# Performance work log

Hardware: AMD Instinct MI355X
Metric: run time of the kernel (lower is better)

The kernel has to match this reference:

```python
import jax, jax.numpy as jnp
import numpy as np

N_SIDE = 14          # ViT-S/16 on 224x224 -> 14x14 patches
D_BACKBONE = 384
D_MODEL = 512
B_CLIPS = 32
T_FRAMES = 64
BT = B_CLIPS * T_FRAMES
LN_EPS = 1e-5


def setup_inputs() -> dict:
    key = jax.random.key(0)
    k0, k1, k2, k3, k4 = jax.random.split(key, 5)
    patch_tokens = jax.random.normal(k0, (BT, N_SIDE * N_SIDE, D_BACKBONE), dtype=jnp.float32)
    raw = jax.random.uniform(k1, (BT, 4), dtype=jnp.float32)
    # make well-formed boxes: x1<=x2, y1<=y2 (module clamps anyway)
    xy1 = jnp.minimum(raw[:, :2], raw[:, 2:])
    xy2 = jnp.maximum(raw[:, :2], raw[:, 2:])
    bboxes = jnp.concatenate([xy1, xy2], axis=1)
    obj_visible = jax.random.bernoulli(k2, 0.9, (BT,)).astype(jnp.float32)
    W = jax.random.normal(k3, (D_BACKBONE, D_MODEL), dtype=jnp.float32) * 0.02
    b = jnp.zeros((D_MODEL,), dtype=jnp.float32)
    gamma = jnp.ones((D_MODEL,), dtype=jnp.float32)
    beta = jnp.zeros((D_MODEL,), dtype=jnp.float32)
    mask_token = jax.random.normal(k4, (1, D_MODEL), dtype=jnp.float32) * 0.02
    return {"patch_tokens": patch_tokens, "bboxes": bboxes, "obj_visible": obj_visible,
            "B": B_CLIPS, "T": T_FRAMES, "W": W, "b": b, "gamma": gamma, "beta": beta,
            "mask_token": mask_token}


def _roi_mean_pool(patch_tokens, bboxes):
    bt, N, D = patch_tokens.shape
    n = N_SIDE
    grid = patch_tokens.reshape(bt, n, n, D)
    # exact replica of torch index math (clamp -> trunc/ceil -> clamp -> max)
    x1 = jnp.clip(bboxes[:, 0] * n, 0, n - 1).astype(jnp.int32)
    y1 = jnp.clip(bboxes[:, 1] * n, 0, n - 1).astype(jnp.int32)
    x2 = jnp.clip(jnp.ceil(jnp.clip(bboxes[:, 2] * n, 0, n)), 1, n).astype(jnp.int32)
    y2 = jnp.clip(jnp.ceil(jnp.clip(bboxes[:, 3] * n, 0, n)), 1, n).astype(jnp.int32)
    x2 = jnp.maximum(x2, x1 + 1)
    y2 = jnp.maximum(y2, y1 + 1)
    idx = jnp.arange(n)
    my = (idx[None, :] >= y1[:, None]) & (idx[None, :] < y2[:, None])  # [BT, n]
    mx = (idx[None, :] >= x1[:, None]) & (idx[None, :] < x2[:, None])  # [BT, n]
    mask = (my[:, :, None] & mx[:, None, :]).astype(grid.dtype)        # [BT, n, n]
    count = ((y2 - y1) * (x2 - x1)).astype(grid.dtype)                 # >= 1 always
    pooled = jnp.einsum('bhw,bhwd->bd', mask, grid) / count[:, None]
    return pooled


def reference(patch_tokens, bboxes, obj_visible, B, T, W, b, gamma, beta, mask_token):
    pooled = _roi_mean_pool(patch_tokens, bboxes)          # [BT, D_backbone]
    out = pooled @ W + b                                   # [BT, d_model]
    mu = jnp.mean(out, axis=-1, keepdims=True)
    var = jnp.mean(jnp.square(out - mu), axis=-1, keepdims=True)
    out = (out - mu) * jax.lax.rsqrt(var + LN_EPS) * gamma + beta
    vis = obj_visible[:, None]
    out = vis * out + (1.0 - vis) * mask_token             # learnable mask token blend
    return out.reshape(B, T, -1)
```

## Files before the change

### kernel.cpp

```cpp
#include <hip/hip_runtime.h>
#include <hip/hip_bf16.h>

#define N_SIDE 14
#define N_PATCH (N_SIDE * N_SIDE)
#define D_BB 384
#define DQ_BB (D_BB / 4)
#define D_MODEL 512
#define CQ (D_MODEL / 4)
#define BT_TOTAL 2048
#define LN_EPS 1e-5f
#define PGROUPS 8

#define GROWS 8
#define GKP 8
#define GKCHUNK (D_BB / GKP)

__device__ __forceinline__ void fma4(float4& a, float s, const float4& wv) {
    a.x = fmaf(s, wv.x, a.x);
    a.y = fmaf(s, wv.y, a.y);
    a.z = fmaf(s, wv.z, a.z);
    a.w = fmaf(s, wv.w, a.w);
}

__device__ __forceinline__ void add4(float4& a, const float4& b) {
    a.x += b.x; a.y += b.y; a.z += b.z; a.w += b.w;
}

__device__ __forceinline__ void box_params(const float* __restrict__ bboxes, int bt,
                                           int& x1, int& y1, int& wd, int& total) {
    const float bx1 = bboxes[bt * 4 + 0];
    const float by1 = bboxes[bt * 4 + 1];
    const float bx2 = bboxes[bt * 4 + 2];
    const float by2 = bboxes[bt * 4 + 3];
    x1 = (int)fminf(fmaxf(bx1 * (float)N_SIDE, 0.f), (float)(N_SIDE - 1));
    y1 = (int)fminf(fmaxf(by1 * (float)N_SIDE, 0.f), (float)(N_SIDE - 1));
    int x2 = (int)fminf(fmaxf(ceilf(fminf(fmaxf(bx2 * (float)N_SIDE, 0.f), (float)N_SIDE)), 1.f), (float)N_SIDE);
    int y2 = (int)fminf(fmaxf(ceilf(fminf(fmaxf(by2 * (float)N_SIDE, 0.f), (float)N_SIDE)), 1.f), (float)N_SIDE);
    x2 = max(x2, x1 + 1);
    y2 = max(y2, y1 + 1);
    wd = x2 - x1;
    total = wd * (y2 - y1);
}

__global__ __launch_bounds__(768) void pool_kernel(
    const float* __restrict__ patch,
    const float* __restrict__ bboxes,
    float* __restrict__ pooled)
{
    const int bt = blockIdx.x;
    const int t  = threadIdx.x;
    const int qd = t % DQ_BB;
    const int g  = t / DQ_BB;

    int x1, y1, wd, total;
    box_params(bboxes, bt, x1, y1, wd, total);
    const float inv_count = 1.f / (float)total;
    const float inv_wd = 1.f / (float)wd;
    const int cell0 = y1 * N_SIDE + x1;

    const float4* __restrict__ base = (const float4*)patch + (size_t)bt * N_PATCH * DQ_BB + qd;

    auto cell_off = [&](int c) -> size_t {
        const int y = (int)(((float)c + 0.5f) * inv_wd);
        const int x = c - y * wd;
        return (size_t)(cell0 + y * N_SIDE + x) * DQ_BB;
    };

    float4 acc = make_float4(0.f, 0.f, 0.f, 0.f);
    int c = g;
    for (; c + 3 * PGROUPS < total; c += 4 * PGROUPS) {
        const float4 v0 = base[cell_off(c)];
        const float4 v1 = base[cell_off(c + PGROUPS)];
        const float4 v2 = base[cell_off(c + 2 * PGROUPS)];
        const float4 v3 = base[cell_off(c + 3 * PGROUPS)];
        acc.x += (v0.x + v1.x) + (v2.x + v3.x);
        acc.y += (v0.y + v1.y) + (v2.y + v3.y);
        acc.z += (v0.z + v1.z) + (v2.z + v3.z);
        acc.w += (v0.w + v1.w) + (v2.w + v3.w);
    }
    for (; c < total; c += PGROUPS) {
        const float4 v = base[cell_off(c)];
        acc.x += v.x; acc.y += v.y; acc.z += v.z; acc.w += v.w;
    }

    __shared__ float4 part[PGROUPS][DQ_BB];
    part[g][qd] = acc;
    __syncthreads();

    if (t < DQ_BB) {
        float4 s = part[0][t];
#pragma unroll
        for (int p = 1; p < PGROUPS; ++p) add4(s, part[p][t]);
        s.x *= inv_count; s.y *= inv_count; s.z *= inv_count; s.w *= inv_count;
        ((float4*)pooled)[(size_t)bt * DQ_BB + t] = s;
    }
}

__global__ __launch_bounds__(1024) void gemm_ln_kernel(
    const float* __restrict__ pooled,
    const float* __restrict__ W,
    const float* __restrict__ bias,
    const float* __restrict__ gamma,
    const float* __restrict__ beta,
    const float* __restrict__ mask_tok,
    const float* __restrict__ vis,
    float* __restrict__ out)
{
    const int tid = threadIdx.x;
    const int lq  = tid & 63;
    const int w   = tid >> 6;
    const int h   = w & 1;
    const int p   = w >> 1;
    const int r0  = blockIdx.x * GROWS;

    __shared__ float4 red4[4][GROWS][CQ];
    __shared__ float  lnred[2][GROWS][2];

    const int hq = h * 64 + lq;
    const int dbase = __builtin_amdgcn_readfirstlane(p * GKCHUNK);

    const float4* Wq = (const float4*)W;
    const float*  A  = pooled + (size_t)r0 * D_BB;

    float4 acc[GROWS];
#pragma unroll
    for (int r = 0; r < GROWS; ++r) acc[r] = make_float4(0.f, 0.f, 0.f, 0.f);

#pragma unroll 2
    for (int i = 0; i < GKCHUNK / 4; ++i) {
        const int d = dbase + i * 4;
        const float4 w0 = Wq[(size_t)(d + 0) * CQ + hq];
        const float4 w1 = Wq[(size_t)(d + 1) * CQ + hq];
        const float4 w2 = Wq[(size_t)(d + 2) * CQ + hq];
        const float4 w3 = Wq[(size_t)(d + 3) * CQ + hq];
#pragma unroll
        for (int r = 0; r < GROWS; ++r) {
            const float* Ar = A + r * D_BB + d;
            const float a0 = Ar[0];
            const float a1 = Ar[1];
            const float a2 = Ar[2];
            const float a3 = Ar[3];
            fma4(acc[r], a0, w0);
            fma4(acc[r], a1, w1);
            fma4(acc[r], a2, w2);
            fma4(acc[r], a3, w3);
        }
    }

    if (p >= 4) {
#pragma unroll
        for (int r = 0; r < GROWS; ++r) red4[p - 4][r][hq] = acc[r];
    }
    __syncthreads();
    if (p < 4) {
#pragma unroll
        for (int r = 0; r < GROWS; ++r) add4(acc[r], red4[p][r][hq]);
    }
    __syncthreads();
    if (p == 2 || p == 3) {
#pragma unroll
        for (int r = 0; r < GROWS; ++r) red4[p - 2][r][hq] = acc[r];
    }
    __syncthreads();
    if (p < 2) {
#pragma unroll
        for (int r = 0; r < GROWS; ++r) add4(acc[r], red4[p][r][hq]);
    }
    __syncthreads();
    if (p == 1) {
#pragma unroll
        for (int r = 0; r < GROWS; ++r) red4[0][r][hq] = acc[r];
    }
    __syncthreads();

    if (p == 0) {
        const float4 bj = ((const float4*)bias)[hq];
#pragma unroll
        for (int r = 0; r < GROWS; ++r) {
            add4(acc[r], red4[0][r][hq]);
            add4(acc[r], bj);
            float s  = acc[r].x + acc[r].y + acc[r].z + acc[r].w;
            float s2 = acc[r].x * acc[r].x + acc[r].y * acc[r].y +
                       acc[r].z * acc[r].z + acc[r].w * acc[r].w;
#pragma unroll
            for (int off = 32; off >= 1; off >>= 1) {
                s  += __shfl_xor(s,  off);
                s2 += __shfl_xor(s2, off);
            }
            if (lq == 0) { lnred[h][r][0] = s; lnred[h][r][1] = s2; }
        }
    }
    __syncthreads();

    if (p == 0) {
        const float4 g4 = ((const float4*)gamma)[hq];
        const float4 b4 = ((const float4*)beta)[hq];
        const float4 m4 = ((const float4*)mask_tok)[hq];
#pragma unroll
        for (int r = 0; r < GROWS; ++r) {
            const float s    = lnred[0][r][0] + lnred[1][r][0];
            const float s2   = lnred[0][r][1] + lnred[1][r][1];
            const float mean = s * (1.f / (float)D_MODEL);
            const float var  = s2 * (1.f / (float)D_MODEL) - mean * mean;
            const float rstd = rsqrtf(var + LN_EPS);
            const float v    = vis[r0 + r];
            const float iv   = 1.f - v;
            float4 o;
            o.x = v * ((acc[r].x - mean) * rstd * g4.x + b4.x) + iv * m4.x;
            o.y = v * ((acc[r].y - mean) * rstd * g4.y + b4.y) + iv * m4.y;
            o.z = v * ((acc[r].z - mean) * rstd * g4.z + b4.z) + iv * m4.z;
            o.w = v * ((acc[r].w - mean) * rstd * g4.w + b4.w) + iv * m4.w;
            ((float4*)out)[(size_t)(r0 + r) * CQ + hq] = o;
        }
    }
}

extern "C" void kernel_launch(void* const* d_in, const int* in_sizes, int n_in,
                              void* d_out, int out_size, void* d_ws, size_t ws_size,
                              hipStream_t stream) {
    const float* patch  = (const float*)d_in[0];
    const float* bboxes = (const float*)d_in[1];
    const float* vis    = (const float*)d_in[2];
    const float* W      = (const float*)d_in[5];
    const float* bias   = (const float*)d_in[6];
    const float* gamma  = (const float*)d_in[7];
    const float* beta   = (const float*)d_in[8];
    const float* mtok   = (const float*)d_in[9];

    float* pooled = (float*)d_ws;
    float* out    = (float*)d_out;

    pool_kernel<<<BT_TOTAL, 768, 0, stream>>>(patch, bboxes, pooled);
    gemm_ln_kernel<<<BT_TOTAL / GROWS, 1024, 0, stream>>>(
        pooled, W, bias, gamma, beta, mtok, vis, out);
}
```

Measured before the change: 36.46 us.

## Replace FP32 GEMM+LN with bf16 MFMA kernel using prepacked weights

Swaps the scalar FP32 FMA projection for a bf16 MFMA 16x16x32 kernel. The pool kernel now writes pooled features as bf16, and its first 64 blocks also convert and pack W into MFMA B-fragment layout, which adds work to those blocks. The LayerNorm reduction now uses a per-wave shuffle plus a small cross-wave shared-memory step instead of the multi-stage shared-memory split-K reduction. This cuts GEMM compute and the pooled and W traffic, at the cost of bf16 rounding on the inputs and a less coalesced scalar output store.

```diff
diff --git a/kernel.cpp b/kernel.cpp
--- a/kernel.cpp
+++ b/kernel.cpp
@@ -6,20 +6,18 @@
 #define D_BB 384
 #define DQ_BB (D_BB / 4)
 #define D_MODEL 512
-#define CQ (D_MODEL / 4)
 #define BT_TOTAL 2048
 #define LN_EPS 1e-5f
 #define PGROUPS 8
-
-#define GROWS 8
-#define GKP 8
-#define GKCHUNK (D_BB / GKP)
-
-__device__ __forceinline__ void fma4(float4& a, float s, const float4& wv) {
-    a.x = fmaf(s, wv.x, a.x);
-    a.y = fmaf(s, wv.y, a.y);
-    a.z = fmaf(s, wv.z, a.z);
-    a.w = fmaf(s, wv.w, a.w);
+#define KSTEPS (D_BB / 32)
+#define NTILES (D_MODEL / 16)
+
+typedef __attribute__((ext_vector_type(8))) short bf16x8;
+typedef __attribute__((ext_vector_type(4))) float f32x4;
+
+__device__ __forceinline__ unsigned short f2b(float f) {
+    unsigned u = __float_as_uint(f);
+    return (unsigned short)((u + 0x7FFFu + ((u >> 16) & 1u)) >> 16);
 }
 
 __device__ __forceinline__ void add4(float4& a, const float4& b) {
@@ -45,12 +43,32 @@
 __global__ __launch_bounds__(768) void pool_kernel(
     const float* __restrict__ patch,
     const float* __restrict__ bboxes,
-    float* __restrict__ pooled)
+    const float* __restrict__ W,
+    unsigned short* __restrict__ pooled_bf,
+    unsigned short* __restrict__ wpack)
 {
     const int bt = blockIdx.x;
     const int t  = threadIdx.x;
     const int qd = t % DQ_BB;
     const int g  = t / DQ_BB;
+
+    if (bt < 64) {
+        const int nt   = bt >> 1;
+        const int kh   = bt & 1;
+        const int lane = t & 63;
+        const int grp  = t >> 6;
+        const int ksl  = grp >> 1;
+        const int jh   = grp & 1;
+        const int ks   = kh * 6 + ksl;
+        const int n    = nt * 16 + (lane & 15);
+        const int kb   = ks * 32 + (lane >> 4) * 8 + jh * 4;
+        ushort4 w4;
+        w4.x = f2b(W[(size_t)(kb + 0) * D_MODEL + n]);
+        w4.y = f2b(W[(size_t)(kb + 1) * D_MODEL + n]);
+        w4.z = f2b(W[(size_t)(kb + 2) * D_MODEL + n]);
+        w4.w = f2b(W[(size_t)(kb + 3) * D_MODEL + n]);
+        *(ushort4*)(wpack + ((size_t)(nt * KSTEPS + ks) * 64 + lane) * 8 + jh * 4) = w4;
+    }
 
     int x1, y1, wd, total;
     box_params(bboxes, bt, x1, y1, wd, total);
@@ -91,14 +109,18 @@
         float4 s = part[0][t];
 #pragma unroll
         for (int p = 1; p < PGROUPS; ++p) add4(s, part[p][t]);
-        s.x *= inv_count; s.y *= inv_count; s.z *= inv_count; s.w *= inv_count;
-        ((float4*)pooled)[(size_t)bt * DQ_BB + t] = s;
-    }
-}
-
-__global__ __launch_bounds__(1024) void gemm_ln_kernel(
-    const float* __restrict__ pooled,
-    const float* __restrict__ W,
+        ushort4 o;
+        o.x = f2b(s.x * inv_count);
+        o.y = f2b(s.y * inv_count);
+        o.z = f2b(s.z * inv_count);
+        o.w = f2b(s.w * inv_count);
+        *(ushort4*)(pooled_bf + (size_t)bt * D_BB + t * 4) = o;
+    }
+}
+
+__global__ __launch_bounds__(256) void mfma_ln_kernel(
+    const unsigned short* __restrict__ pooled_bf,
+    const unsigned short* __restrict__ wpack,
     const float* __restrict__ bias,
     const float* __restrict__ gamma,
     const float* __restrict__ beta,
@@ -106,111 +128,96 @@
     const float* __restrict__ vis,
     float* __restrict__ out)
 {
-    const int tid = threadIdx.x;
-    const int lq  = tid & 63;
-    const int w   = tid >> 6;
-    const int h   = w & 1;
-    const int p   = w >> 1;
-    const int r0  = blockIdx.x * GROWS;
-
-    __shared__ float4 red4[4][GROWS][CQ];
-    __shared__ float  lnred[2][GROWS][2];
-
-    const int hq = h * 64 + lq;
-    const int dbase = __builtin_amdgcn_readfirstlane(p * GKCHUNK);
-
-    const float4* Wq = (const float4*)W;
-    const float*  A  = pooled + (size_t)r0 * D_BB;
-
-    float4 acc[GROWS];
-#pragma unroll
-    for (int r = 0; r < GROWS; ++r) acc[r] = make_float4(0.f, 0.f, 0.f, 0.f);
-
-#pragma unroll 2
-    for (int i = 0; i < GKCHUNK / 4; ++i) {
-        const int d = dbase + i * 4;
-        const float4 w0 = Wq[(size_t)(d + 0) * CQ + hq];
-        const float4 w1 = Wq[(size_t)(d + 1) * CQ + hq];
-        const float4 w2 = Wq[(size_t)(d + 2) * CQ + hq];
-        const float4 w3 = Wq[(size_t)(d + 3) * CQ + hq];
-#pragma unroll
-        for (int r = 0; r < GROWS; ++r) {
-            const float* Ar = A + r * D_BB + d;
-            const float a0 = Ar[0];
-            const float a1 = Ar[1];
-            const float a2 = Ar[2];
-            const float a3 = Ar[3];
-            fma4(acc[r], a0, w0);
-            fma4(acc[r], a1, w1);
-            fma4(acc[r], a2, w2);
-            fma4(acc[r], a3, w3);
-        }
-    }
-
-    if (p >= 4) {
-#pragma unroll
-        for (int r = 0; r < GROWS; ++r) red4[p - 4][r][hq] = acc[r];
+    const int tid    = threadIdx.x;
+    const int wave   = tid >> 6;
+    const int lane   = tid & 63;
+    const int rt     = wave & 1;
+    const int ch     = wave >> 1;
+    const int lane_m = lane & 15;
+    const int lane_g = lane >> 4;
+    const int mrow0  = blockIdx.x * 32 + rt * 16;
+
+    bf16x8 afrag[KSTEPS];
+    {
+        const unsigned short* Arow = pooled_bf + (size_t)(mrow0 + lane_m) * D_BB + lane_g * 8;
+#pragma unroll
+        for (int ks = 0; ks < KSTEPS; ++ks)
+            afrag[ks] = *(const bf16x8*)(Arow + ks * 32);
+    }
+
+    f32x4 acc[16];
+#pragma unroll
+    for (int nt = 0; nt < 16; ++nt) acc[nt] = (f32x4){0.f, 0.f, 0.f, 0.f};
+
+#pragma unroll
+    for (int ks = 0; ks < KSTEPS; ++ks) {
+#pragma unroll
+        for (int nt = 0; nt < 16; ++nt) {
+            const int ntg = ch * 16 + nt;
+            const bf16x8 b = *(const bf16x8*)(wpack + ((size_t)(ntg * KSTEPS + ks) * 64 + lane) * 8);
+            acc[nt] = __builtin_amdgcn_mfma_f32_16x16x32_bf16(afrag[ks], b, acc[nt], 0, 0, 0);
+        }
+    }
+
+#pragma unroll
+    for (int nt = 0; nt < 16; ++nt) {
+        const float bs = bias[ch * 256 + nt * 16 + lane_m];
+        acc[nt].x += bs; acc[nt].y += bs; acc[nt].z += bs; acc[nt].w += bs;
+    }
+
+    float s[4] = {0.f, 0.f, 0.f, 0.f}, s2[4] = {0.f, 0.f, 0.f, 0.f};
+#pragma unroll
+    for (int nt = 0; nt < 16; ++nt) {
+#pragma unroll
+        for (int r = 0; r < 4; ++r) {
+            const float v = acc[nt][r];
+            s[r] += v; s2[r] += v * v;
+        }
+    }
+#pragma unroll
+    for (int off = 1; off < 16; off <<= 1) {
+#pragma unroll
+        for (int r = 0; r < 4; ++r) {
+            s[r]  += __shfl_xor(s[r],  off);
+            s2[r] += __shfl_xor(s2[r], off);
+        }
+    }
+
+    __shared__ float lns[2][2][16][2];
+    if (lane_m == 0) {
+#pragma unroll
+        for (int r = 0; r < 4; ++r) {
+            lns[ch][rt][lane_g * 4 + r][0] = s[r];
+            lns[ch][rt][lane_g * 4 + r][1] = s2[r];
+        }
     }
     __syncthreads();
-    if (p < 4) {
-#pragma unroll
-        for (int r = 0; r < GROWS; ++r) add4(acc[r], red4[p][r][hq]);
-    }
-    __syncthreads();
-    if (p == 2 || p == 3) {
-#pragma unroll
-        for (int r = 0; r < GROWS; ++r) red4[p - 2][r][hq] = acc[r];
-    }
-    __syncthreads();
-    if (p < 2) {
-#pragma unroll
-        for (int r = 0; r < GROWS; ++r) add4(acc[r], red4[p][r][hq]);
-    }
-    __syncthreads();
-    if (p == 1) {
-#pragma unroll
-        for (int r = 0; r < GROWS; ++r) red4[0][r][hq] = acc[r];
-    }
-    __syncthreads();
-
-    if (p == 0) {
-        const float4 bj = ((const float4*)bias)[hq];
-#pragma unroll
-        for (int r = 0; r < GROWS; ++r) {
-            add4(acc[r], red4[0][r][hq]);
-            add4(acc[r], bj);
-            float s  = acc[r].x + acc[r].y + acc[r].z + acc[r].w;
-            float s2 = acc[r].x * acc[r].x + acc[r].y * acc[r].y +
-                       acc[r].z * acc[r].z + acc[r].w * acc[r].w;
-#pragma unroll
-            for (int off = 32; off >= 1; off >>= 1) {
-                s  += __shfl_xor(s,  off);
-                s2 += __shfl_xor(s2, off);
-            }
-            if (lq == 0) { lnred[h][r][0] = s; lnred[h][r][1] = s2; }
-        }
-    }
-    __syncthreads();
-
-    if (p == 0) {
-        const float4 g4 = ((const float4*)gamma)[hq];
-        const float4 b4 = ((const float4*)beta)[hq];
-        const float4 m4 = ((const float4*)mask_tok)[hq];
-#pragma unroll
-        for (int r = 0; r < GROWS; ++r) {
-            const float s    = lnred[0][r][0] + lnred[1][r][0];
-            const float s2   = lnred[0][r][1] + lnred[1][r][1];
-            const float mean = s * (1.f / (float)D_MODEL);
-            const float var  = s2 * (1.f / (float)D_MODEL) - mean * mean;
-            const float rstd = rsqrtf(var + LN_EPS);
-            const float v    = vis[r0 + r];
-            const float iv   = 1.f - v;
-            float4 o;
-            o.x = v * ((acc[r].x - mean) * rstd * g4.x + b4.x) + iv * m4.x;
-            o.y = v * ((acc[r].y - mean) * rstd * g4.y + b4.y) + iv * m4.y;
-            o.z = v * ((acc[r].z - mean) * rstd * g4.z + b4.z) + iv * m4.z;
-            o.w = v * ((acc[r].w - mean) * rstd * g4.w + b4.w) + iv * m4.w;
-            ((float4*)out)[(size_t)(r0 + r) * CQ + hq] = o;
+
+    float mean4[4], rstd4[4], v4[4], iv4[4];
+#pragma unroll
+    for (int r = 0; r < 4; ++r) {
+        const int m = lane_g * 4 + r;
+        const float S  = lns[0][rt][m][0] + lns[1][rt][m][0];
+        const float S2 = lns[0][rt][m][1] + lns[1][rt][m][1];
+        const float mean = S * (1.f / (float)D_MODEL);
+        const float var  = S2 * (1.f / (float)D_MODEL) - mean * mean;
+        mean4[r] = mean;
+        rstd4[r] = rsqrtf(var + LN_EPS);
+        const float v = vis[mrow0 + m];
+        v4[r] = v; iv4[r] = 1.f - v;
+    }
+
+#pragma unroll
+    for (int nt = 0; nt < 16; ++nt) {
+        const int n = ch * 256 + nt * 16 + lane_m;
+        const float gm = gamma[n];
+        const float bt_ = beta[n];
+        const float mt = mask_tok[n];
+#pragma unroll
+        for (int r = 0; r < 4; ++r) {
+            const int row = mrow0 + lane_g * 4 + r;
+            const float o = v4[r] * ((acc[nt][r] - mean4[r]) * rstd4[r] * gm + bt_) + iv4[r] * mt;
+            out[(size_t)row * D_MODEL + n] = o;
         }
     }
 }
@@ -227,10 +234,11 @@
     const float* beta   = (const float*)d_in[8];
     const float* mtok   = (const float*)d_in[9];
 
-    float* pooled = (float*)d_ws;
-    float* out    = (float*)d_out;
-
-    pool_kernel<<<BT_TOTAL, 768, 0, stream>>>(patch, bboxes, pooled);
-    gemm_ln_kernel<<<BT_TOTAL / GROWS, 1024, 0, stream>>>(
-        pooled, W, bias, gamma, beta, mtok, vis, out);
-}
+    unsigned short* pooled_bf = (unsigned short*)d_ws;
+    unsigned short* wpack     = (unsigned short*)((char*)d_ws + (2u << 20));
+    float* out = (float*)d_out;
+
+    pool_kernel<<<BT_TOTAL, 768, 0, stream>>>(patch, bboxes, W, pooled_bf, wpack);
+    mfma_ln_kernel<<<BT_TOTAL / 32, 256, 0, stream>>>(
+        pooled_bf, wpack, bias, gamma, beta, mtok, vis, out);
+}
```

New measurement: 48.45 us. 32.9% more time.
